# Kernel tuning notes

Hardware: AMD Instinct MI355X
Metric: run time of the kernel (lower is better)

The kernel has to match this reference:

```python
import jax, jax.numpy as jnp
import numpy as np

N_SEGMENT = 8  # frames per clip
N_DIV = 8      # fold divisor: fold = C // N_DIV channels shift each way


def setup_inputs() -> dict:
    key = jax.random.key(0)
    k1, k2 = jax.random.split(key)
    x = jax.random.normal(k1, (128, 256, 28, 28), dtype=jnp.float32)  # [nt, C, H, W], nt = 16 clips * 8 frames
    net_weight = jax.random.normal(k2, (256, 256), dtype=jnp.float32) * 0.0625  # 1x1 conv [out_c, in_c]
    return {"x": x, "net_weight": net_weight}


def temporal_shift(x):
    # x: [nt, C, H, W]. Equivalent to the fixed one-hot depthwise Conv3d (k=3, pad=1):
    #   channels [:fold]        -> out[t] = x[t-1]  (weight[...,0]=1)
    #   channels [fold:2*fold]  -> out[t] = x[t+1]  (weight[...,2]=1)
    #   channels [2*fold:]      -> out[t] = x[t]    (weight[...,1]=1)
    nt, c, h, w = x.shape
    b = nt // N_SEGMENT
    xv = x.reshape(b, N_SEGMENT, c, h, w)
    fold = c // N_DIV
    prev = jnp.pad(xv[:, :-1, :fold], ((0, 0), (1, 0), (0, 0), (0, 0), (0, 0)))       # shift right in time
    nxt = jnp.pad(xv[:, 1:, fold:2 * fold], ((0, 0), (0, 1), (0, 0), (0, 0), (0, 0)))  # shift left in time
    shifted = jnp.concatenate([prev, nxt, xv[:, :, 2 * fold:]], axis=2)
    return shifted.reshape(nt, c, h, w)


def reference(x, net_weight):
    y = temporal_shift(x)
    # wrapped net: 1x1 Conv2d(256 -> 256, bias=False) == per-pixel GEMM
    out = jnp.einsum('nchw,oc->nohw', y, net_weight)
    return out
```

## Files before the change

kernel.cpp:

```cpp
#include <hip/hip_runtime.h>
#include <hip/hip_bf16.h>


#define N_FRAMES 8
#define C_DIM    256
#define HW       784
#define P_TILE   112
#define FOLD     32
#define LDS_STRIDE 264

using bf16x8 = __attribute__((ext_vector_type(8))) short;
using f32x4  = __attribute__((ext_vector_type(4))) float;

static __device__ __forceinline__ unsigned int pk2(float lo, float hi) {
    union { __hip_bfloat162 h; unsigned int u; } cv;
    cv.h = __float22bfloat162_rn(make_float2(lo, hi));
    return cv.u;
}

static __device__ __forceinline__ unsigned short bf1(float v) {
    union { __hip_bfloat16 h; unsigned short u; } cv;
    cv.h = __float2bfloat16(v);
    return cv.u;
}

__global__ __launch_bounds__(512, 4)
void tsm_pw_gemm(const float* __restrict__ x,
                 const float* __restrict__ w,
                 float* __restrict__ out) {
    __shared__ __align__(16) unsigned short ylds[P_TILE * LDS_STRIDE];

    const int n    = blockIdx.x;
    const int tile = blockIdx.y;
    const int p0   = tile * P_TILE;
    const int tid  = threadIdx.x;
    const int tf   = n & (N_FRAMES - 1);

    f32x4 vals[14];
    int   cs[14], pvs[14];
    #pragma unroll
    for (int i = 0; i < 14; ++i) {
        const int vidx = tid + i * 512;
        const int c  = vidx / 28;
        const int pv = vidx - c * 28;
        cs[i] = c; pvs[i] = pv;
        int  nsrc;
        bool valid;
        if (c < FOLD)           { nsrc = n - 1; valid = (tf > 0); }
        else if (c < 2 * FOLD)  { nsrc = n + 1; valid = (tf < N_FRAMES - 1); }
        else                    { nsrc = n;     valid = true; }
        const float* src = x + ((size_t)(valid ? nsrc : n) * C_DIM + c) * HW
                             + p0 + pv * 4;
        f32x4 v = {0.f, 0.f, 0.f, 0.f};
        if (valid) v = *(const f32x4*)src;
        vals[i] = v;
    }
    #pragma unroll
    for (int i = 0; i < 14; ++i) {
        const int c  = cs[i];
        const int pv = pvs[i];
        const int cc = c ^ ((pv & 7) << 3);
        const int rb = pv * 4 * LDS_STRIDE + cc;
        ylds[rb                 ] = bf1(vals[i][0]);
        ylds[rb + 1 * LDS_STRIDE] = bf1(vals[i][1]);
        ylds[rb + 2 * LDS_STRIDE] = bf1(vals[i][2]);
        ylds[rb + 3 * LDS_STRIDE] = bf1(vals[i][3]);
    }
    __syncthreads();

    const int lane = tid & 63;
    const int wv   = tid >> 6;
    const int g    = lane >> 4;
    const int ol   = lane & 15;

    f32x4 acc[2][7];
    #pragma unroll
    for (int m = 0; m < 2; ++m)
        #pragma unroll
        for (int nn = 0; nn < 7; ++nn)
            acc[m][nn] = f32x4{0.f, 0.f, 0.f, 0.f};

    for (int kk = 0; kk < 8; ++kk) {
        const int c = kk * 32 + g * 8;
        bf16x8 af[2];
        #pragma unroll
        for (int m = 0; m < 2; ++m) {
            const int o = wv * 32 + m * 16 + ol;
            const float* wp = w + (size_t)o * C_DIM + c;
            f32x4 w0 = *(const f32x4*)wp;
            f32x4 w1 = *(const f32x4*)(wp + 4);
            union { bf16x8 v; unsigned int u4[4]; } cv;
            cv.u4[0] = pk2(w0[0], w0[1]);
            cv.u4[1] = pk2(w0[2], w0[3]);
            cv.u4[2] = pk2(w1[0], w1[1]);
            cv.u4[3] = pk2(w1[2], w1[3]);
            af[m] = cv.v;
        }
        #pragma unroll
        for (int nn = 0; nn < 7; ++nn) {
            const int p  = nn * 16 + ol;
            const int cc = c ^ (((p >> 2) & 7) << 3);
            const bf16x8 bfrag = *(const bf16x8*)&ylds[p * LDS_STRIDE + cc];
            #pragma unroll
            for (int m = 0; m < 2; ++m)
                acc[m][nn] = __builtin_amdgcn_mfma_f32_16x16x32_bf16(
                    af[m], bfrag, acc[m][nn], 0, 0, 0);
        }
    }

    const size_t outbase = (size_t)n * C_DIM * HW + p0 + ol;
    #pragma unroll
    for (int m = 0; m < 2; ++m) {
        #pragma unroll
        for (int r = 0; r < 4; ++r) {
            const int o = wv * 32 + m * 16 + g * 4 + r;
            float* orow = out + outbase + (size_t)o * HW;
            #pragma unroll
            for (int nn = 0; nn < 7; ++nn)
                orow[nn * 16] = acc[m][nn][r];
        }
    }
}

extern "C" void kernel_launch(void* const* d_in, const int* in_sizes, int n_in,
                              void* d_out, int out_size, void* d_ws, size_t ws_size,
                              hipStream_t stream) {
    const float* x = (const float*)d_in[0];
    const float* w = (const float*)d_in[1];
    float* out     = (float*)d_out;
    dim3 grid(128, 7, 1);
    tsm_pw_gemm<<<grid, dim3(512, 1, 1), 0, stream>>>(x, w, out);
}
```

Measured before the change: 57.35 us.

## Pre-convert weights to bf16 and pack channel pairs into LDS stores

A small pre-kernel converts the weight matrix to bf16 in workspace, so the GEMM kernel loads ready bf16 fragments instead of re-reading and converting fp32 weights in every block. The activation staging now loads two adjacent channels per thread and writes packed 32-bit bf16 pairs to LDS, halving the number of LDS store instructions. It also fully unrolls the k loop and adds a scheduling barrier between the loads and the LDS stores. The extra kernel launch adds a little fixed overhead, and the fallback path keeps the old behaviour when no workspace is available.

```diff
diff --git a/kernel.cpp b/kernel.cpp
--- a/kernel.cpp
+++ b/kernel.cpp
@@ -18,15 +18,19 @@
     return cv.u;
 }
 
-static __device__ __forceinline__ unsigned short bf1(float v) {
-    union { __hip_bfloat16 h; unsigned short u; } cv;
-    cv.h = __float2bfloat16(v);
-    return cv.u;
+__global__ void wconv(const float* __restrict__ w, unsigned short* __restrict__ wb) {
+    const int i = (blockIdx.x * 256 + threadIdx.x) * 4;
+    f32x4 v = *(const f32x4*)(w + i);
+    unsigned int lo = pk2(v[0], v[1]);
+    unsigned int hi = pk2(v[2], v[3]);
+    *(uint2*)(wb + i) = make_uint2(lo, hi);
 }
 
+template <bool USE_WB>
 __global__ __launch_bounds__(512, 4)
 void tsm_pw_gemm(const float* __restrict__ x,
                  const float* __restrict__ w,
+                 const unsigned short* __restrict__ wb,
                  float* __restrict__ out) {
     __shared__ __align__(16) unsigned short ylds[P_TILE * LDS_STRIDE];
 
@@ -36,35 +40,40 @@
     const int tid  = threadIdx.x;
     const int tf   = n & (N_FRAMES - 1);
 
-    f32x4 vals[14];
-    int   cs[14], pvs[14];
+    f32x4 v0[7], v1[7];
+    int   cps[7], pvs[7];
     #pragma unroll
-    for (int i = 0; i < 14; ++i) {
-        const int vidx = tid + i * 512;
-        const int c  = vidx / 28;
-        const int pv = vidx - c * 28;
-        cs[i] = c; pvs[i] = pv;
+    for (int i = 0; i < 7; ++i) {
+        const int idx = tid + i * 512;
+        const int cp  = idx / 28;
+        const int pv  = idx - cp * 28;
+        cps[i] = cp; pvs[i] = pv;
+        const int c0 = cp * 2;
         int  nsrc;
         bool valid;
-        if (c < FOLD)           { nsrc = n - 1; valid = (tf > 0); }
-        else if (c < 2 * FOLD)  { nsrc = n + 1; valid = (tf < N_FRAMES - 1); }
-        else                    { nsrc = n;     valid = true; }
-        const float* src = x + ((size_t)(valid ? nsrc : n) * C_DIM + c) * HW
+        if (c0 < FOLD)           { nsrc = n - 1; valid = (tf > 0); }
+        else if (c0 < 2 * FOLD)  { nsrc = n + 1; valid = (tf < N_FRAMES - 1); }
+        else                     { nsrc = n;     valid = true; }
+        const float* src = x + ((size_t)(valid ? nsrc : n) * C_DIM + c0) * HW
                              + p0 + pv * 4;
-        f32x4 v = {0.f, 0.f, 0.f, 0.f};
-        if (valid) v = *(const f32x4*)src;
-        vals[i] = v;
+        f32x4 a = {0.f, 0.f, 0.f, 0.f};
+        f32x4 b = {0.f, 0.f, 0.f, 0.f};
+        if (valid) {
+            a = *(const f32x4*)src;
+            b = *(const f32x4*)(src + HW);
+        }
+        v0[i] = a; v1[i] = b;
     }
+    __builtin_amdgcn_sched_barrier(0);
     #pragma unroll
-    for (int i = 0; i < 14; ++i) {
-        const int c  = cs[i];
+    for (int i = 0; i < 7; ++i) {
+        const int c0 = cps[i] * 2;
         const int pv = pvs[i];
-        const int cc = c ^ ((pv & 7) << 3);
+        const int cc = c0 ^ ((pv & 7) << 3);
         const int rb = pv * 4 * LDS_STRIDE + cc;
-        ylds[rb                 ] = bf1(vals[i][0]);
-        ylds[rb + 1 * LDS_STRIDE] = bf1(vals[i][1]);
-        ylds[rb + 2 * LDS_STRIDE] = bf1(vals[i][2]);
-        ylds[rb + 3 * LDS_STRIDE] = bf1(vals[i][3]);
+        #pragma unroll
+        for (int r = 0; r < 4; ++r)
+            *(unsigned int*)&ylds[rb + r * LDS_STRIDE] = pk2(v0[i][r], v1[i][r]);
     }
     __syncthreads();
 
@@ -80,21 +89,26 @@
         for (int nn = 0; nn < 7; ++nn)
             acc[m][nn] = f32x4{0.f, 0.f, 0.f, 0.f};
 
+    #pragma unroll
     for (int kk = 0; kk < 8; ++kk) {
         const int c = kk * 32 + g * 8;
         bf16x8 af[2];
         #pragma unroll
         for (int m = 0; m < 2; ++m) {
             const int o = wv * 32 + m * 16 + ol;
-            const float* wp = w + (size_t)o * C_DIM + c;
-            f32x4 w0 = *(const f32x4*)wp;
-            f32x4 w1 = *(const f32x4*)(wp + 4);
-            union { bf16x8 v; unsigned int u4[4]; } cv;
-            cv.u4[0] = pk2(w0[0], w0[1]);
-            cv.u4[1] = pk2(w0[2], w0[3]);
-            cv.u4[2] = pk2(w1[0], w1[1]);
-            cv.u4[3] = pk2(w1[2], w1[3]);
-            af[m] = cv.v;
+            if (USE_WB) {
+                af[m] = *(const bf16x8*)&wb[(size_t)o * C_DIM + c];
+            } else {
+                const float* wp = w + (size_t)o * C_DIM + c;
+                f32x4 w0 = *(const f32x4*)wp;
+                f32x4 w1 = *(const f32x4*)(wp + 4);
+                union { bf16x8 v; unsigned int u4[4]; } cv;
+                cv.u4[0] = pk2(w0[0], w0[1]);
+                cv.u4[1] = pk2(w0[2], w0[3]);
+                cv.u4[2] = pk2(w1[0], w1[1]);
+                cv.u4[3] = pk2(w1[2], w1[3]);
+                af[m] = cv.v;
+            }
         }
         #pragma unroll
         for (int nn = 0; nn < 7; ++nn) {
@@ -129,5 +143,11 @@
     const float* w = (const float*)d_in[1];
     float* out     = (float*)d_out;
     dim3 grid(128, 7, 1);
-    tsm_pw_gemm<<<grid, dim3(512, 1, 1), 0, stream>>>(x, w, out);
+    if (ws_size >= (size_t)C_DIM * C_DIM * sizeof(unsigned short)) {
+        unsigned short* wb = (unsigned short*)d_ws;
+        wconv<<<64, 256, 0, stream>>>(w, wb);
+        tsm_pw_gemm<true><<<grid, dim3(512, 1, 1), 0, stream>>>(x, w, wb, out);
+    } else {
+        tsm_pw_gemm<false><<<grid, dim3(512, 1, 1), 0, stream>>>(x, w, nullptr, out);
+    }
 }
```

Result: faster. 52.32 us (-8.8%).
